# Performance work log

Hardware: AMD Instinct MI355X
Metric: run time of the kernel (lower is better)

The kernel has to match this reference:

```python
import jax, jax.numpy as jnp
import numpy as np

B, T, IN, U, OUT = 64, 256, 256, 768, 64


def setup_inputs() -> dict:
    key = jax.random.key(0)
    ks = jax.random.split(key, 4)
    s = 0.05  # small init scale to keep gates in a sane range
    return {
        "x": jax.random.normal(ks[0], (B, T, IN), jnp.float32),
        # keras GRU kernel: [input_dim, 3*units], gate order (z, r, h)
        "kernel": jax.random.normal(ks[1], (IN, 3 * U), jnp.float32) * s,
        "rec_kernel": jax.random.normal(ks[2], (U, 3 * U), jnp.float32) * s,
        # reset_after=True bias: row 0 = input bias, row 1 = recurrent bias; init ones
        "bias": jnp.ones((2, 3 * U), jnp.float32),
        "w_out": jax.random.normal(ks[3], (U, OUT), jnp.float32) * s,
        "b_out": jnp.ones((OUT,), jnp.float32),
    }


def reference(x, kernel, rec_kernel, bias, w_out, b_out):
    # keras GRU, reset_after=True, activation='relu', recurrent_activation='sigmoid',
    # return_sequences=False -> last hidden state only; then Dense (linear).
    units = rec_kernel.shape[0]
    b_in, b_rec = bias[0], bias[1]
    # Precompute all input projections in one big GEMM: [B, T, 3U]
    xp = jnp.einsum("bti,ih->bth", x, kernel) + b_in
    xz, xr, xh = jnp.split(xp, 3, axis=-1)

    def step(h, xs):
        xz_t, xr_t, xh_t = xs  # each [B, U]
        inner = h @ rec_kernel + b_rec  # [B, 3U]
        iz, ir, ih = jnp.split(inner, 3, axis=-1)
        z = jax.nn.sigmoid(xz_t + iz)
        r = jax.nn.sigmoid(xr_t + ir)
        hh = jax.nn.relu(xh_t + r * ih)  # reset_after: r applied AFTER rec matmul
        h_new = z * h + (1.0 - z) * hh
        return h_new, None

    h0 = jnp.zeros((x.shape[0], units), x.dtype)
    xs = (jnp.swapaxes(xz, 0, 1), jnp.swapaxes(xr, 0, 1), jnp.swapaxes(xh, 0, 1))
    h_last, _ = jax.lax.scan(step, h0, xs)
    return h_last @ w_out + b_out  # Dense with linear activation
```

## Files before the change

### kernel.cpp

```cpp
#include <hip/hip_runtime.h>

#define B_   64
#define T_   256
#define IN_  256
#define U_   768
#define C3_  2304
#define OUT_ 64
#define NWG  24
#define NTH  384

#define ARR_OFF     0u
#define ARR_BYTES   0x20000u
#define RING_OFF    0x20000u
#define SLOT_STRIDE 98304u
#define RING_BYTES  ((size_t)(T_ + 1) * SLOT_STRIDE)
#define XFRAG_OFF   0x1880000u
#define XFRAG_BYTES ((size_t)T_ * 2 * 16 * 1024)
#define WS_NEED     ((size_t)XFRAG_OFF + XFRAG_BYTES)

typedef __bf16 bf16x8 __attribute__((ext_vector_type(8)));
typedef float  f32x16 __attribute__((ext_vector_type(16)));
typedef int    i32x4  __attribute__((ext_vector_type(4)));

__device__ __forceinline__ unsigned short f2bf(float f) {
  unsigned u = __float_as_uint(f);
  u += 0x7fff + ((u >> 16) & 1);
  return (unsigned short)(u >> 16);
}
__device__ __forceinline__ unsigned pkbf(float lo, float hi) {
  unsigned r;
  asm volatile("v_cvt_pk_bf16_f32 %0, %1, %2" : "=v"(r) : "v"(lo), "v"(hi));
  return r;
}

#define BYPASS_LOAD(dst, src) \
  asm volatile("global_load_dwordx4 %0, %1, off sc0 sc1" : "=v"(dst) : "v"(src))
#define PLAIN_LOAD(dst, src) \
  asm volatile("global_load_dwordx4 %0, %1, off" : "=v"(dst) : "v"(src))
#define BYPASS_STORE(dst, val) \
  asm volatile("global_store_dwordx4 %0, %1, off sc0 sc1" :: "v"(dst), "v"(val) : "memory")
#define WAITV8 do { asm volatile("s_waitcnt vmcnt(8)" ::: "memory"); \
                    __builtin_amdgcn_sched_barrier(0); } while (0)
#define WAITV0 do { asm volatile("s_waitcnt vmcnt(0)" ::: "memory"); \
                    __builtin_amdgcn_sched_barrier(0); } while (0)

#define ISSUE8(BUF, KB) do { \
  _Pragma("unroll") \
  for (int i_ = 0; i_ < 8; ++i_) \
    PLAIN_LOAD(BUF[i_], pbase + ((KB) + i_) * 1024); \
} while (0)

#define MFMA8(BUF, KB) do { \
  _Pragma("unroll") \
  for (int i_ = 0; i_ < 8; ++i_) { \
    bf16x8 av_ = wbase[((KB) + i_) * 64]; \
    accA = __builtin_amdgcn_mfma_f32_32x32x16_bf16( \
        av_, __builtin_bit_cast(bf16x8, BUF[i_]), accA, 0, 0, 0); \
  } \
} while (0)

__global__ void __launch_bounds__(256) prep_xfrag(
    const float* __restrict__ x, void* __restrict__ wsv)
{
  __shared__ float xls[64][264];
  const int t   = blockIdx.x;
  const int tid = threadIdx.x;
  const int l   = tid & 63;
  const int w   = tid >> 6;
  const int ln  = l & 31, lh = l >> 5;
  {
    const int row = tid >> 2, cb = (tid & 3) * 64;
    const float* src = x + (size_t)row * T_ * IN_ + (size_t)t * IN_ + cb;
    #pragma unroll
    for (int q = 0; q < 16; ++q)
      *(float4*)&xls[row][cb + q * 4] = *(const float4*)(src + q * 4);
  }
  __syncthreads();
  #pragma unroll
  for (int s = 0; s < 8; ++s) {
    const int idx = w * 8 + s, mt = idx >> 4, kk = idx & 15;
    const float* p = &xls[mt * 32 + ln][kk * 16 + lh * 8];
    union { bf16x8 v; unsigned u[4]; i32x4 q; } a;
    a.u[0] = pkbf(p[0], p[1]); a.u[1] = pkbf(p[2], p[3]);
    a.u[2] = pkbf(p[4], p[5]); a.u[3] = pkbf(p[6], p[7]);
    *(i32x4*)((char*)wsv + XFRAG_OFF
              + (size_t)((t * 2 + mt) * 16 + kk) * 1024 + (size_t)l * 16) = a.q;
  }
}

__global__ void __launch_bounds__(NTH, 2) gru_mfma(
    const float* __restrict__ x, const float* __restrict__ kern,
    const float* __restrict__ rec, const float* __restrict__ bias,
    const float* __restrict__ w_out, const float* __restrict__ b_out,
    float* __restrict__ out, void* __restrict__ wsv)
{
  unsigned* arrive = (unsigned*)((char*)wsv + ARR_OFF);
  char*     ring   = (char*)wsv + RING_OFF;

  __shared__ bf16x8  recF[3 * 48 * 64];
  __shared__ unsigned exch[2][2][64][9];

  const int tid = threadIdx.x;
  const int l   = tid & 63;
  const int j   = __builtin_amdgcn_readfirstlane(tid >> 6);
  const int mt  = j & 1;
  const int g   = j >> 1;
  const int wg  = blockIdx.x;
  const int u0  = wg * 32;
  const int ln  = l & 31;
  const int lh  = l >> 5;
  const bool lo = (l < 32);
  const int wcol = g * U_ + u0 + ln;

  for (int kk = mt * 24; kk < mt * 24 + 24; ++kk) {
    union { bf16x8 v; unsigned short s[8]; } fr;
    #pragma unroll
    for (int i = 0; i < 8; ++i)
      fr.s[i] = f2bf(rec[(size_t)(kk * 16 + lh * 8 + i) * C3_ + wcol]);
    recF[(g * 48 + kk) * 64 + l] = fr.v;
  }
  bf16x8 xkern[16];
  #pragma unroll
  for (int kk = 0; kk < 16; ++kk) {
    union { bf16x8 v; unsigned short s[8]; } fr;
    #pragma unroll
    for (int i = 0; i < 8; ++i)
      fr.s[i] = f2bf(kern[(size_t)(kk * 16 + lh * 8 + i) * C3_ + wcol]);
    xkern[kk] = fr.v;
  }

  f32x16 vbiasA, vbiasX;
  #pragma unroll
  for (int r = 0; r < 16; ++r) {
    int u = u0 + (r & 3) + 8 * (r >> 2) + 4 * lh;
    if (g < 2) { vbiasA[r] = bias[g * U_ + u] + bias[C3_ + g * U_ + u]; vbiasX[r] = 0.f; }
    else       { vbiasA[r] = bias[C3_ + 2 * U_ + u]; vbiasX[r] = bias[2 * U_ + u]; }
  }

  float hown[16];
  #pragma unroll
  for (int i = 0; i < 16; ++i) hown[i] = 0.f;

  const bf16x8* wbase = &recF[(g * 48) * 64 + l];
  const char*   xfrg  = (const char*)wsv + XFRAG_OFF + (size_t)l * 16;
  __syncthreads();

  for (int t = 0; t < T_; ++t) {
    f32x16 accA = vbiasA;
    f32x16 accX = vbiasX;

    {
      const char* xfb = xfrg + (size_t)((t * 2 + mt) * 16) * 1024;
      #pragma unroll
      for (int kk = 0; kk < 16; ++kk) {
        bf16x8 bv = *(const bf16x8*)(xfb + (size_t)kk * 1024);
        accX = __builtin_amdgcn_mfma_f32_32x32x16_bf16(xkern[kk], bv, accX, 0, 0, 0);
      }
    }

    if (t > 0) {
      const unsigned* ap = arrive + ((size_t)t * 2 + mt) * 32;
      while (__hip_atomic_load(ap, __ATOMIC_RELAXED, __HIP_MEMORY_SCOPE_AGENT) < NWG)
        __builtin_amdgcn_s_sleep(1);
      WAITV0;

      const char* pbase = ring + (size_t)t * SLOT_STRIDE
                        + (size_t)mt * (48 * 1024) + (size_t)l * 16;
      i32x4 h0b[8], h1b[8];
      ISSUE8(h0b, 0);  ISSUE8(h1b, 8);
      WAITV8; MFMA8(h0b, 0);  ISSUE8(h0b, 16);
      WAITV8; MFMA8(h1b, 8);  ISSUE8(h1b, 24);
      WAITV8; MFMA8(h0b, 16); ISSUE8(h0b, 32);
      WAITV8; MFMA8(h1b, 24); ISSUE8(h1b, 40);
      WAITV8; MFMA8(h0b, 32);
      WAITV0; MFMA8(h1b, 40);
    }

    if (g < 2) {
      f32x16 pre = accA + accX;
      #pragma unroll
      for (int i = 0; i < 8; ++i)
        exch[mt][g][l][i] = pkbf(pre[2 * i], pre[2 * i + 1]);
    }
    __syncthreads();

    unsigned zw[8], rw[8];
    if (g == 2) {
      #pragma unroll
      for (int i = 0; i < 8; ++i) { zw[i] = exch[mt][0][l][i]; rw[i] = exch[mt][1][l][i]; }
    }
    __syncthreads();

    if (g == 2) {
      f32x16 crec = accA;
      float hn[16];
      #pragma unroll
      for (int i = 0; i < 8; ++i) {
        float zf[2] = { __uint_as_float(zw[i] << 16), __uint_as_float(zw[i] & 0xffff0000u) };
        float rf[2] = { __uint_as_float(rw[i] << 16), __uint_as_float(rw[i] & 0xffff0000u) };
        #pragma unroll
        for (int e = 0; e < 2; ++e) {
          const int r = 2 * i + e;
          float z  = 1.f / (1.f + __expf(-zf[e]));
          float rr = 1.f / (1.f + __expf(-rf[e]));
          float hh = fmaxf(0.f, accX[r] + rr * crec[r]);
          float h  = z * hown[r] + (1.f - z) * hh;
          hown[r] = h; hn[r] = h;
        }
      }
      int w0 = (int)pkbf(hn[0],  hn[1]),  w1 = (int)pkbf(hn[2],  hn[3]);
      int w2 = (int)pkbf(hn[4],  hn[5]),  w3 = (int)pkbf(hn[6],  hn[7]);
      int w4 = (int)pkbf(hn[8],  hn[9]),  w5 = (int)pkbf(hn[10], hn[11]);
      int w6 = (int)pkbf(hn[12], hn[13]), w7 = (int)pkbf(hn[14], hn[15]);
      int sx0 = __shfl_xor(w0, 32, 64), sx1 = __shfl_xor(w1, 32, 64);
      int sx2 = __shfl_xor(w2, 32, 64), sx3 = __shfl_xor(w3, 32, 64);
      int sx4 = __shfl_xor(w4, 32, 64), sx5 = __shfl_xor(w5, 32, 64);
      int sx6 = __shfl_xor(w6, 32, 64), sx7 = __shfl_xor(w7, 32, 64);
      i32x4 f0, f1;
      f0[0] = lo ? w0 : sx2;  f0[1] = lo ? w1 : sx3;
      f0[2] = lo ? sx0 : w2;  f0[3] = lo ? sx1 : w3;
      f1[0] = lo ? w4 : sx6;  f1[1] = lo ? w5 : sx7;
      f1[2] = lo ? sx4 : w6;  f1[3] = lo ? sx5 : w7;

      char* dstb = ring + (size_t)(t + 1) * SLOT_STRIDE
                 + (size_t)(mt * 48 + 2 * wg) * 1024 + (size_t)l * 16;
      BYPASS_STORE(dstb, f0);
      BYPASS_STORE(dstb + 1024, f1);
      asm volatile("s_waitcnt vmcnt(0)" ::: "memory");
      if (l == 0)
        __hip_atomic_fetch_add(arrive + ((size_t)(t + 1) * 2 + mt) * 32, 1u,
                               __ATOMIC_RELAXED, __HIP_MEMORY_SCOPE_AGENT);
    }
  }

  if (wg < 16) {
    const unsigned* a0 = arrive + ((size_t)T_ * 2 + 0) * 32;
    const unsigned* a1 = arrive + ((size_t)T_ * 2 + 1) * 32;
    while (__hip_atomic_load(a0, __ATOMIC_RELAXED, __HIP_MEMORY_SCOPE_AGENT) < NWG ||
           __hip_atomic_load(a1, __ATOMIC_RELAXED, __HIP_MEMORY_SCOPE_AGENT) < NWG)
      __builtin_amdgcn_s_sleep(2);
    asm volatile("" ::: "memory");

    unsigned short* hrow = (unsigned short*)recF;
    {
      const int blocal = tid / 96, c = tid % 96;
      const int kk = c >> 1, lhh = c & 1;
      const int b = wg * 4 + blocal, mtb = b >> 5, lnb = b & 31;
      const char* src = ring + (size_t)T_ * SLOT_STRIDE
                      + (size_t)(mtb * 48 + kk) * 1024 + (size_t)(lhh * 32 + lnb) * 16;
      i32x4 v;
      BYPASS_LOAD(v, src);
      asm volatile("s_waitcnt vmcnt(0)" ::: "memory");
      *(i32x4*)&hrow[blocal * 768 + kk * 16 + lhh * 8] = v;
    }
    __syncthreads();
    if (j < 4) {
      const int b = wg * 4 + j;
      float acc = 0.f;
      #pragma unroll 8
      for (int k = 0; k < U_; ++k)
        acc += __uint_as_float((unsigned)hrow[j * 768 + k] << 16)
             * w_out[(size_t)k * OUT_ + l];
      out[(size_t)b * OUT_ + l] = acc + b_out[l];
    }
  }
}

extern "C" void kernel_launch(void* const* d_in, const int* in_sizes, int n_in,
                              void* d_out, int out_size, void* d_ws, size_t ws_size,
                              hipStream_t stream) {
  const float* x     = (const float*)d_in[0];
  const float* kern  = (const float*)d_in[1];
  const float* rec   = (const float*)d_in[2];
  const float* bias  = (const float*)d_in[3];
  const float* w_out = (const float*)d_in[4];
  const float* b_out = (const float*)d_in[5];
  float* outp = (float*)d_out;
  void* wsv   = d_ws;

  if (ws_size < WS_NEED) return;

  hipMemsetAsync(d_ws, 0, ARR_BYTES, stream);
  prep_xfrag<<<T_, 256, 0, stream>>>(x, d_ws);

  void* args[] = {(void*)&x, (void*)&kern, (void*)&rec, (void*)&bias,
                  (void*)&w_out, (void*)&b_out, (void*)&outp, (void*)&wsv};
  hipLaunchCooperativeKernel(reinterpret_cast<void*>(&gru_mfma),
                             dim3(NWG), dim3(NTH), args, 0u, stream);
}
```

Before: 1.963 ms.

## Place all persistent workgroups on one XCC and drop cache-bypass ring accesses

The kernel now launches 256 workgroups. Each reads its hardware XCC id and claims a ticket with an atomic counter per XCC. The first XCC to gather 24 workgroups wins, and only those 24 keep running with roles from their tickets; the rest exit. With every worker on one XCC sharing an L2, the per-step hidden-state ring stores and the final loads switch from sc0/sc1 bypass to plain accesses, cutting cross-XCC coherence latency in the serial recurrence. The risks are correctness if plain stores do not become visible in time through the shared L2, the wasted launch of extra blocks, and reliance on undocumented hardware register encoding.

```diff
diff --git a/kernel.cpp b/kernel.cpp
--- a/kernel.cpp
+++ b/kernel.cpp
@@ -8,9 +8,11 @@
 #define OUT_ 64
 #define NWG  24
 #define NTH  384
+#define GRID 256
 
 #define ARR_OFF     0u
 #define ARR_BYTES   0x20000u
+#define CLAIM_OFF   0x18000u
 #define RING_OFF    0x20000u
 #define SLOT_STRIDE 98304u
 #define RING_BYTES  ((size_t)(T_ + 1) * SLOT_STRIDE)
@@ -18,6 +20,8 @@
 #define XFRAG_BYTES ((size_t)T_ * 2 * 16 * 1024)
 #define WS_NEED     ((size_t)XFRAG_OFF + XFRAG_BYTES)
 
+#define XCC_GETREG_IMM ((31 << 11) | (0 << 6) | 20)
+
 typedef __bf16 bf16x8 __attribute__((ext_vector_type(8)));
 typedef float  f32x16 __attribute__((ext_vector_type(16)));
 typedef int    i32x4  __attribute__((ext_vector_type(4)));
@@ -33,12 +37,10 @@
   return r;
 }
 
-#define BYPASS_LOAD(dst, src) \
-  asm volatile("global_load_dwordx4 %0, %1, off sc0 sc1" : "=v"(dst) : "v"(src))
 #define PLAIN_LOAD(dst, src) \
   asm volatile("global_load_dwordx4 %0, %1, off" : "=v"(dst) : "v"(src))
-#define BYPASS_STORE(dst, val) \
-  asm volatile("global_store_dwordx4 %0, %1, off sc0 sc1" :: "v"(dst), "v"(val) : "memory")
+#define PLAIN_STORE(dst, val) \
+  asm volatile("global_store_dwordx4 %0, %1, off" :: "v"(dst), "v"(val) : "memory")
 #define WAITV8 do { asm volatile("s_waitcnt vmcnt(8)" ::: "memory"); \
                     __builtin_amdgcn_sched_barrier(0); } while (0)
 #define WAITV0 do { asm volatile("s_waitcnt vmcnt(0)" ::: "memory"); \
@@ -95,17 +97,38 @@
     float* __restrict__ out, void* __restrict__ wsv)
 {
   unsigned* arrive = (unsigned*)((char*)wsv + ARR_OFF);
+  unsigned* claim  = (unsigned*)((char*)wsv + CLAIM_OFF);
   char*     ring   = (char*)wsv + RING_OFF;
 
   __shared__ bf16x8  recF[3 * 48 * 64];
   __shared__ unsigned exch[2][2][64][9];
+  __shared__ unsigned s_role;
+
+  if (threadIdx.x == 0) {
+    unsigned xcc = __builtin_amdgcn_s_getreg(XCC_GETREG_IMM) & 7u;
+    unsigned tk = __hip_atomic_fetch_add(&claim[xcc], 1u,
+                                         __ATOMIC_RELAXED, __HIP_MEMORY_SCOPE_AGENT);
+    if (tk == 23u) {
+      unsigned exp = 0u;
+      __hip_atomic_compare_exchange_strong(&claim[16], &exp, xcc + 1u,
+          __ATOMIC_RELAXED, __ATOMIC_RELAXED, __HIP_MEMORY_SCOPE_AGENT);
+    }
+    unsigned w;
+    while ((w = __hip_atomic_load(&claim[16], __ATOMIC_RELAXED,
+                                  __HIP_MEMORY_SCOPE_AGENT)) == 0u)
+      __builtin_amdgcn_s_sleep(2);
+    s_role = (xcc == w - 1u && tk < 24u) ? tk : 0xFFFFFFFFu;
+  }
+  __syncthreads();
+  const unsigned role = s_role;
+  if (role == 0xFFFFFFFFu) return;
 
   const int tid = threadIdx.x;
   const int l   = tid & 63;
   const int j   = __builtin_amdgcn_readfirstlane(tid >> 6);
   const int mt  = j & 1;
   const int g   = j >> 1;
-  const int wg  = blockIdx.x;
+  const int wg  = (int)role;
   const int u0  = wg * 32;
   const int ln  = l & 31;
   const int lh  = l >> 5;
@@ -224,8 +247,8 @@
 
       char* dstb = ring + (size_t)(t + 1) * SLOT_STRIDE
                  + (size_t)(mt * 48 + 2 * wg) * 1024 + (size_t)l * 16;
-      BYPASS_STORE(dstb, f0);
-      BYPASS_STORE(dstb + 1024, f1);
+      PLAIN_STORE(dstb, f0);
+      PLAIN_STORE(dstb + 1024, f1);
       asm volatile("s_waitcnt vmcnt(0)" ::: "memory");
       if (l == 0)
         __hip_atomic_fetch_add(arrive + ((size_t)(t + 1) * 2 + mt) * 32, 1u,
@@ -249,7 +272,7 @@
       const char* src = ring + (size_t)T_ * SLOT_STRIDE
                       + (size_t)(mtb * 48 + kk) * 1024 + (size_t)(lhh * 32 + lnb) * 16;
       i32x4 v;
-      BYPASS_LOAD(v, src);
+      PLAIN_LOAD(v, src);
       asm volatile("s_waitcnt vmcnt(0)" ::: "memory");
       *(i32x4*)&hrow[blocal * 768 + kk * 16 + lhh * 8] = v;
     }
@@ -286,5 +309,5 @@
   void* args[] = {(void*)&x, (void*)&kern, (void*)&rec, (void*)&bias,
                   (void*)&w_out, (void*)&b_out, (void*)&outp, (void*)&wsv};
   hipLaunchCooperativeKernel(reinterpret_cast<void*>(&gru_mfma),
-                             dim3(NWG), dim3(NTH), args, 0u, stream);
-}
+                             dim3(GRID), dim3(NTH), args, 0u, stream);
+}
```

After: 1.957 ms. About the same (-0.3%).
